# Kernel tuning notes

Hardware: AMD Instinct MI355X
Metric: run time of the kernel (lower is better)

The kernel has to match this reference:

```python
import jax, jax.numpy as jnp
import numpy as np

T, D = 1024, 1024            # tokens, model dim
E, K = 16, 4                 # routed experts, top-k
G, TG = 4, 2                 # expert groups, limited (top) groups
INTER = 512                  # moe_inter_dim
SHARED_INTER = 2 * INTER     # n_shared_experts * moe_inter_dim
ROUTE_SCALE = 2.5
STD = 0.02


def setup_inputs() -> dict:
    key = jax.random.key(0)
    ks = jax.random.split(key, 9)
    return {
        "x": jax.random.normal(ks[0], (T, D), jnp.float32),
        "token_mask": jnp.ones((T,), jnp.bool_),
        "gate_w": jax.random.normal(ks[1], (E, D), jnp.float32) * STD,
        "gate_bias": jnp.zeros((E,), jnp.float32),  # e_score_correction_bias (zero-init)
        "gate_projs": jax.random.normal(ks[2], (E, INTER, D), jnp.float32) * STD,
        "up_projs": jax.random.normal(ks[3], (E, INTER, D), jnp.float32) * STD,
        "down_projs": jax.random.normal(ks[4], (E, D, INTER), jnp.float32) * STD,
        "shared_gate": jax.random.normal(ks[5], (SHARED_INTER, D), jnp.float32) * STD,
        "shared_up": jax.random.normal(ks[6], (SHARED_INTER, D), jnp.float32) * STD,
        "shared_down": jax.random.normal(ks[7], (D, SHARED_INTER), jnp.float32) * STD,
    }


def _route(x, gate_w, gate_bias):
    # sigmoid scoring with e_score_correction_bias + group-limited top-k (DeepSeek-V3 style)
    scores = jax.nn.sigmoid(x @ gate_w.T)                      # [T, E]
    s = (scores + gate_bias).reshape(T, G, E // G)             # bias-corrected, grouped
    group_scores = jax.lax.top_k(s, 2)[0].sum(-1)              # [T, G] sum of top-2 per group
    gidx = jax.lax.top_k(group_scores, TG)[1]                  # [T, TG]
    gmask = jax.nn.one_hot(gidx, G, dtype=s.dtype).sum(1)      # [T, G] selected-group mask
    masked = (s * gmask[:, :, None]).reshape(T, E)
    idx = jax.lax.top_k(masked, K)[1]                          # [T, K] expert indices
    w = jnp.take_along_axis(scores, idx, axis=1)               # gather original (unbiased) scores
    w = w / w.sum(-1, keepdims=True) * ROUTE_SCALE             # sigmoid renorm + route scale
    return w.astype(x.dtype), idx


def reference(x, token_mask, gate_w, gate_bias, gate_projs, up_projs,
              down_projs, shared_gate, shared_up, shared_down):
    w, idx = _route(x, gate_w, gate_bias)
    # dense combine weights [T, E]: combine[t, e] = sum_k w[t, k] * (idx[t, k] == e)
    combine = (jax.nn.one_hot(idx, E, dtype=x.dtype) * w[..., None]).sum(1)

    def body(acc, p):
        gp, up, dp, c = p                                      # per-expert SwiGLU
        inter = jax.nn.silu(x @ gp.T) * (x @ up.T)             # [T, INTER]
        return acc + c[:, None] * (inter @ dp.T), None

    routed, _ = jax.lax.scan(
        body, jnp.zeros_like(x), (gate_projs, up_projs, down_projs, combine.T))
    shared = (jax.nn.silu(x @ shared_gate.T) * (x @ shared_up.T)) @ shared_down.T
    return routed + shared
```

## Files before the change

kernel.cpp:

```cpp
#include <hip/hip_runtime.h>
#include <stdint.h>

#define TTOK 1024
#define DMODEL 1024
#define NEXP 16
#define TOPK 4
#define INTER 512
#define NSHI 1024
#define RSCALE 2.5f

typedef __bf16 bf16;
typedef __bf16 bf16x8 __attribute__((ext_vector_type(8)));
typedef __bf16 bf16x4 __attribute__((ext_vector_type(4)));
typedef float f32x4 __attribute__((ext_vector_type(4)));

#define APLANE 2064
#define BPLANE 1040

__global__ __launch_bounds__(256)
void scores_kernel(const float* __restrict__ x, const float* __restrict__ gw,
                   float* __restrict__ scores, bf16* __restrict__ xbf) {
  __shared__ float gws[16 * 1024];
  const int tid = threadIdx.x;
  const float4* gw4 = (const float4*)gw;
#pragma unroll
  for (int i0 = 0; i0 < 4096; i0 += 256) {
    const int i = i0 + tid;
    const int e = i >> 8;
    const int dq = (i & 255) << 2;
    const int dd = (dq + 4 * e) & 1023;
    ((float4*)gws)[(e << 8) + (dd >> 2)] = gw4[i];
  }
  {
    const long xb = (long)blockIdx.x * 1024;
#pragma unroll
    for (int p = 0; p < 4; ++p) {
      const long j = xb + p * 256 + tid;
      const float4 v = ((const float4*)x)[j];
      bf16x4 o;
      o.x = (bf16)v.x; o.y = (bf16)v.y; o.z = (bf16)v.z; o.w = (bf16)v.w;
      ((bf16x4*)xbf)[j] = o;
    }
  }
  __syncthreads();
  const int kq = tid >> 6;
  const int lane = tid & 63;
  const int tl = lane >> 4;
  const int e = lane & 15;
  const long token = (long)blockIdx.x * 4 + tl;
  float acc = 0.f;
  const int dbase = kq * 256;
#pragma unroll 8
  for (int i = 0; i < 256; i += 4) {
    const int d = dbase + i;
    const float4 xv = *(const float4*)&x[token * DMODEL + d];
    const float4 wv = *(const float4*)&gws[(e << 10) + ((d + 4 * e) & 1023)];
    acc += xv.x * wv.x + xv.y * wv.y + xv.z * wv.z + xv.w * wv.w;
  }
  __syncthreads();
  gws[kq * 64 + lane] = acc;
  __syncthreads();
  if (kq == 0) {
    const float s = gws[lane] + gws[64 + lane] + gws[128 + lane] + gws[192 + lane];
    scores[token * 16 + e] = s;
  }
}

__global__ __launch_bounds__(256)
void topk_kernel(const float* __restrict__ scores, const float* __restrict__ gb,
                 int* __restrict__ tokIdx, float* __restrict__ tokW,
                 int* __restrict__ counts) {
  __shared__ int h[NEXP];
  const int tid = threadIdx.x;
  if (tid < NEXP) h[tid] = 0;
  __syncthreads();
  const int t = blockIdx.x * 256 + tid;
  float sc[NEXP], s[NEXP];
#pragma unroll
  for (int e = 0; e < NEXP; ++e) {
    const float l = scores[t * NEXP + e];
    sc[e] = 1.f / (1.f + expf(-l));
    s[e] = sc[e] + gb[e];
  }
  float gsc[4];
#pragma unroll
  for (int g = 0; g < 4; ++g) {
    const float a = s[4 * g], b = s[4 * g + 1], c = s[4 * g + 2], d = s[4 * g + 3];
    gsc[g] = fmaxf(fmaxf(fmaxf(a + b, a + c), fmaxf(a + d, b + c)),
                   fmaxf(b + d, c + d));
  }
  int g0 = 0;
  for (int g = 1; g < 4; ++g) if (gsc[g] > gsc[g0]) g0 = g;
  int g1 = (g0 == 0) ? 1 : 0;
  for (int g = 0; g < 4; ++g) if (g != g0 && gsc[g] > gsc[g1]) g1 = g;
  float m[NEXP];
#pragma unroll
  for (int e = 0; e < NEXP; ++e) {
    const int g = e >> 2;
    m[e] = (g == g0 || g == g1) ? s[e] : -1.f;
  }
  int idx[TOPK]; float wv[TOPK]; float wsum = 0.f;
  for (int k = 0; k < TOPK; ++k) {
    int am = 0; float best = m[0];
    for (int e2 = 1; e2 < NEXP; ++e2)
      if (m[e2] > best) { best = m[e2]; am = e2; }
    idx[k] = am; wv[k] = sc[am]; wsum += sc[am]; m[am] = -2.f;
  }
  const float scl = RSCALE / wsum;
  for (int k = 0; k < TOPK; ++k) {
    tokIdx[t * TOPK + k] = idx[k];
    tokW[t * TOPK + k] = wv[k] * scl;
    atomicAdd(&h[idx[k]], 1);
  }
  __syncthreads();
  if (tid < NEXP) atomicAdd(&counts[tid], h[tid]);
}

__global__ void plan_kernel(const int* __restrict__ counts, int* __restrict__ offs,
                            int* __restrict__ cursors, int* __restrict__ tileE,
                            int* __restrict__ tileR, int* __restrict__ tileCnt) {
  if (threadIdx.x == 0) {
    int acc = 0;
    for (int e = 0; e < NEXP; ++e) { offs[e] = acc; cursors[e] = acc; acc += counts[e]; }
    offs[NEXP] = acc;
    int tc = 0;
    for (int e = 0; e < NEXP; ++e)
      for (int r = offs[e]; r < offs[e + 1]; r += 128) { tileE[tc] = e; tileR[tc] = r; ++tc; }
    for (int r = 0; r < TTOK; r += 128) { tileE[tc] = NEXP; tileR[tc] = r; ++tc; }
    tileCnt[0] = tc;
  }
}

__global__ __launch_bounds__(256)
void fill_kernel(const int* __restrict__ tokIdx, int* __restrict__ cursors,
                 int* __restrict__ slotTok, int* __restrict__ tokSlot) {
  __shared__ int h[NEXP], base[NEXP];
  const int tid = threadIdx.x;
  if (tid < NEXP) h[tid] = 0;
  __syncthreads();
  const int t = blockIdx.x * 256 + tid;
  int myE[TOPK], myR[TOPK];
#pragma unroll
  for (int k = 0; k < TOPK; ++k) {
    myE[k] = tokIdx[t * TOPK + k];
    myR[k] = atomicAdd(&h[myE[k]], 1);
  }
  __syncthreads();
  if (tid < NEXP) base[tid] = atomicAdd(&cursors[tid], h[tid]);
  __syncthreads();
#pragma unroll
  for (int k = 0; k < TOPK; ++k) {
    const int slot = base[myE[k]] + myR[k];
    slotTok[slot] = t;
    tokSlot[t * TOPK + k] = slot;
  }
}

__global__ __launch_bounds__(256, 2)
void gateup_gemm(const bf16* __restrict__ xbf, const int* __restrict__ slotTok,
                 const int* __restrict__ offs, const int* __restrict__ tileE,
                 const int* __restrict__ tileR, const int* __restrict__ tileCnt,
                 const float* __restrict__ Wg, const float* __restrict__ Wu,
                 const float* __restrict__ Sg, const float* __restrict__ Su,
                 bf16* __restrict__ interR, bf16* __restrict__ interS) {
  const int y = blockIdx.y;
  if (y >= tileCnt[0]) return;
  const int e = tileE[y];
  const bool shd = (e == NEXP);
  const int n0 = blockIdx.x * 64;
  if (!shd && n0 >= INTER) return;
  const int rowStart = tileR[y];
  const int rowEnd = shd ? rowStart + 128 : offs[e + 1];
  const float* wgp = shd ? Sg : Wg + (long)e * INTER * DMODEL;
  const float* wup = shd ? Su : Wu + (long)e * INTER * DMODEL;

  __shared__ __attribute__((aligned(16))) char As[8 * APLANE];
  __shared__ __attribute__((aligned(16))) char Bg[8 * BPLANE];
  __shared__ __attribute__((aligned(16))) char Bu[8 * BPLANE];
  __shared__ int tokS[128];

  const int tid = threadIdx.x;
  if (tid < 128) {
    const int r = rowStart + tid;
    tokS[tid] = shd ? r : slotTok[r < rowEnd ? r : rowStart];
  }
  __syncthreads();

  const int arw = tid >> 3;
  const int aoct = tid & 7;
  const bf16* aSrc[4];
#pragma unroll
  for (int p = 0; p < 4; ++p)
    aSrc[p] = xbf + (long)tokS[p * 32 + arw] * DMODEL + aoct * 8;

  const int bu_ = tid >> 7;
  const int u = tid & 127;
  const int brw = u >> 4;
  const int bf4 = u & 15;
  const int boct = bf4 >> 1;
  const int bhalf = bf4 & 1;
  const float* bSrc = (bu_ ? wup : wgp) + (long)n0 * DMODEL + bf4 * 4;
  char* bDst = bu_ ? Bu : Bg;

  const int lane = tid & 63;
  const int wv = tid >> 6;
  const int q = lane >> 4;
  const int l15 = lane & 15;
  const int wm = (wv >> 1) * 64;
  const int wn = (wv & 1) * 32;

  const f32x4 fz = {0.f, 0.f, 0.f, 0.f};
  f32x4 accG[4][2], accU[4][2];
#pragma unroll
  for (int i = 0; i < 4; ++i)
#pragma unroll
    for (int j = 0; j < 2; ++j) { accG[i][j] = fz; accU[i][j] = fz; }

  bf16x8 av[4];
  float4 bv[8];
#pragma unroll
  for (int p = 0; p < 4; ++p) av[p] = *(const bf16x8*)(aSrc[p]);
#pragma unroll
  for (int p = 0; p < 8; ++p)
    bv[p] = *(const float4*)(bSrc + (long)(p * 8 + brw) * DMODEL);

  for (int k0 = 0; k0 < DMODEL; k0 += 64) {
    __syncthreads();
#pragma unroll
    for (int p = 0; p < 4; ++p)
      *(bf16x8*)(As + aoct * APLANE + (p * 32 + arw) * 16) = av[p];
#pragma unroll
    for (int p = 0; p < 8; ++p) {
      bf16x4 w;
      w.x = (bf16)bv[p].x; w.y = (bf16)bv[p].y; w.z = (bf16)bv[p].z; w.w = (bf16)bv[p].w;
      *(bf16x4*)(bDst + boct * BPLANE + (p * 8 + brw) * 16 + bhalf * 8) = w;
    }
    const int kn = k0 + 64;
    if (kn < DMODEL) {
#pragma unroll
      for (int p = 0; p < 4; ++p) av[p] = *(const bf16x8*)(aSrc[p] + kn);
#pragma unroll
      for (int p = 0; p < 8; ++p)
        bv[p] = *(const float4*)(bSrc + (long)(p * 8 + brw) * DMODEL + kn);
    }
    __syncthreads();
#pragma unroll
    for (int kb = 0; kb < 2; ++kb) {
      bf16x8 aF[4];
#pragma unroll
      for (int mi = 0; mi < 4; ++mi)
        aF[mi] = *(const bf16x8*)(As + (4 * kb + q) * APLANE + (wm + 16 * mi + l15) * 16);
#pragma unroll
      for (int ni = 0; ni < 2; ++ni) {
        const int br = wn + 16 * ni + l15;
        const bf16x8 gF = *(const bf16x8*)(Bg + (4 * kb + q) * BPLANE + br * 16);
        const bf16x8 uF = *(const bf16x8*)(Bu + (4 * kb + q) * BPLANE + br * 16);
#pragma unroll
        for (int mi = 0; mi < 4; ++mi) {
          accG[mi][ni] = __builtin_amdgcn_mfma_f32_16x16x32_bf16(aF[mi], gF, accG[mi][ni], 0, 0, 0);
          accU[mi][ni] = __builtin_amdgcn_mfma_f32_16x16x32_bf16(aF[mi], uF, accU[mi][ni], 0, 0, 0);
        }
      }
    }
  }

  bf16* outI = shd ? interS : interR;
  const int ldI = shd ? NSHI : INTER;
#pragma unroll
  for (int mi = 0; mi < 4; ++mi)
#pragma unroll
    for (int r = 0; r < 4; ++r) {
      const int rowLoc = wm + 16 * mi + q * 4 + r;
      const int row = rowStart + rowLoc;
      if (row < rowEnd) {
#pragma unroll
        for (int ni = 0; ni < 2; ++ni) {
          const float gg = accG[mi][ni][r];
          const float uu = accU[mi][ni][r];
          const float sv = gg / (1.f + __expf(-gg)) * uu;
          outI[(long)row * ldI + (n0 + wn + 16 * ni + l15)] = (bf16)sv;
        }
      }
    }
}

__global__ __launch_bounds__(256, 2)
void down_gemm(const bf16* __restrict__ interR, const bf16* __restrict__ interS,
               const int* __restrict__ offs, const int* __restrict__ tileE,
               const int* __restrict__ tileR, const int* __restrict__ tileCnt,
               const float* __restrict__ Wd, const float* __restrict__ Sd,
               float* __restrict__ dsR, float* __restrict__ dsS) {
  const int y = blockIdx.y;
  if (y >= tileCnt[0]) return;
  const int e = tileE[y];
  const bool shd = (e == NEXP);
  const int n0 = blockIdx.x * 64;
  const int rowStart = tileR[y];
  const int rowEnd = shd ? rowStart + 128 : offs[e + 1];
  const int Kd = shd ? NSHI : INTER;
  const bf16* A = shd ? interS : interR;
  const float* wd = shd ? Sd : Wd + (long)e * DMODEL * INTER;

  __shared__ __attribute__((aligned(16))) char As[8 * APLANE];
  __shared__ __attribute__((aligned(16))) char Bs[8 * BPLANE];

  const int tid = threadIdx.x;
  const int arw = tid >> 3;
  const int aoct = tid & 7;
  const bf16* aSrc[4];
#pragma unroll
  for (int p = 0; p < 4; ++p)
    aSrc[p] = A + (long)(rowStart + p * 32 + arw) * Kd + aoct * 8;

  const int brw = tid >> 4;
  const int bf4 = tid & 15;
  const int boct = bf4 >> 1;
  const int bhalf = bf4 & 1;
  const float* bSrc = wd + (long)n0 * Kd + bf4 * 4;

  const int lane = tid & 63;
  const int wv = tid >> 6;
  const int q = lane >> 4;
  const int l15 = lane & 15;
  const int wm = (wv >> 1) * 64;
  const int wn = (wv & 1) * 32;

  const f32x4 fz = {0.f, 0.f, 0.f, 0.f};
  f32x4 acc[4][2];
#pragma unroll
  for (int i = 0; i < 4; ++i)
#pragma unroll
    for (int j = 0; j < 2; ++j) acc[i][j] = fz;

  bf16x8 av[4];
  float4 bv[4];
#pragma unroll
  for (int p = 0; p < 4; ++p) av[p] = *(const bf16x8*)(aSrc[p]);
#pragma unroll
  for (int p = 0; p < 4; ++p)
    bv[p] = *(const float4*)(bSrc + (long)(p * 16 + brw) * Kd);

  for (int k0 = 0; k0 < Kd; k0 += 64) {
    __syncthreads();
#pragma unroll
    for (int p = 0; p < 4; ++p)
      *(bf16x8*)(As + aoct * APLANE + (p * 32 + arw) * 16) = av[p];
#pragma unroll
    for (int p = 0; p < 4; ++p) {
      bf16x4 w;
      w.x = (bf16)bv[p].x; w.y = (bf16)bv[p].y; w.z = (bf16)bv[p].z; w.w = (bf16)bv[p].w;
      *(bf16x4*)(Bs + boct * BPLANE + (p * 16 + brw) * 16 + bhalf * 8) = w;
    }
    const int kn = k0 + 64;
    if (kn < Kd) {
#pragma unroll
      for (int p = 0; p < 4; ++p) av[p] = *(const bf16x8*)(aSrc[p] + kn);
#pragma unroll
      for (int p = 0; p < 4; ++p)
        bv[p] = *(const float4*)(bSrc + (long)(p * 16 + brw) * Kd + kn);
    }
    __syncthreads();
#pragma unroll
    for (int kb = 0; kb < 2; ++kb) {
      bf16x8 aF[4];
#pragma unroll
      for (int mi = 0; mi < 4; ++mi)
        aF[mi] = *(const bf16x8*)(As + (4 * kb + q) * APLANE + (wm + 16 * mi + l15) * 16);
#pragma unroll
      for (int ni = 0; ni < 2; ++ni) {
        const bf16x8 bF = *(const bf16x8*)(Bs + (4 * kb + q) * BPLANE + (wn + 16 * ni + l15) * 16);
#pragma unroll
        for (int mi = 0; mi < 4; ++mi)
          acc[mi][ni] = __builtin_amdgcn_mfma_f32_16x16x32_bf16(aF[mi], bF, acc[mi][ni], 0, 0, 0);
      }
    }
  }

  float* dst = shd ? dsS : dsR;
#pragma unroll
  for (int mi = 0; mi < 4; ++mi)
#pragma unroll
    for (int r = 0; r < 4; ++r) {
      const int rowLoc = wm + 16 * mi + q * 4 + r;
      const int row = rowStart + rowLoc;
      if (row < rowEnd) {
#pragma unroll
        for (int ni = 0; ni < 2; ++ni)
          dst[(long)row * DMODEL + (n0 + wn + 16 * ni + l15)] = acc[mi][ni][r];
      }
    }
}

__global__ __launch_bounds__(256)
void combine_kernel(const float* __restrict__ dsR, const float* __restrict__ dsS,
                    const int* __restrict__ tokSlot, const float* __restrict__ tokW,
                    float* __restrict__ out) {
  const int t = blockIdx.x;
  const int j = threadIdx.x;
  float4 v = ((const float4*)(dsS + (long)t * DMODEL))[j];
#pragma unroll
  for (int k = 0; k < TOPK; ++k) {
    const int s = tokSlot[t * TOPK + k];
    const float w = tokW[t * TOPK + k];
    const float4 r = ((const float4*)(dsR + (long)s * DMODEL))[j];
    v.x += w * r.x; v.y += w * r.y; v.z += w * r.z; v.w += w * r.w;
  }
  ((float4*)(out + (long)t * DMODEL))[j] = v;
}

extern "C" void kernel_launch(void* const* d_in, const int* in_sizes, int n_in,
                              void* d_out, int out_size, void* d_ws, size_t ws_size,
                              hipStream_t stream) {
  const float* x  = (const float*)d_in[0];
  const float* gw = (const float*)d_in[2];
  const float* gb = (const float*)d_in[3];
  const float* gp = (const float*)d_in[4];
  const float* up = (const float*)d_in[5];
  const float* dp = (const float*)d_in[6];
  const float* sg = (const float*)d_in[7];
  const float* su = (const float*)d_in[8];
  const float* sd = (const float*)d_in[9];
  float* out = (float*)d_out;

  char* base = (char*)d_ws;
  size_t off = 0;
  auto alloc = [&](size_t bytes) -> char* {
    off = (off + 255) & ~(size_t)255;
    char* p = base + off;
    off += bytes;
    return p;
  };
  bf16* xbf = (bf16*)alloc((size_t)TTOK * DMODEL * 2);
  bf16* interR = (bf16*)alloc((size_t)(TTOK * TOPK + 128) * INTER * 2);
  bf16* interS = (bf16*)alloc((size_t)TTOK * NSHI * 2);
  float* dsR = (float*)alloc((size_t)TTOK * TOPK * DMODEL * 4);
  float* dsS = (float*)alloc((size_t)TTOK * DMODEL * 4);
  float* scores = (float*)alloc((size_t)TTOK * NEXP * 4);
  int* tokIdx = (int*)alloc(TTOK * TOPK * 4);
  float* tokW = (float*)alloc(TTOK * TOPK * 4);
  int* slotTok = (int*)alloc(TTOK * TOPK * 4);
  int* tokSlot = (int*)alloc(TTOK * TOPK * 4);
  int* counts = (int*)alloc(NEXP * 4);
  int* offs = (int*)alloc((NEXP + 1) * 4);
  int* cursors = (int*)alloc(NEXP * 4);
  int* tileE = (int*)alloc(72 * 4);
  int* tileR = (int*)alloc(72 * 4);
  int* tileCnt = (int*)alloc(4);

  hipMemsetAsync(counts, 0, NEXP * 4, stream);

  scores_kernel<<<TTOK / 4, 256, 0, stream>>>(x, gw, scores, xbf);
  topk_kernel<<<TTOK / 256, 256, 0, stream>>>(scores, gb, tokIdx, tokW, counts);
  plan_kernel<<<1, 64, 0, stream>>>(counts, offs, cursors, tileE, tileR, tileCnt);
  fill_kernel<<<TTOK / 256, 256, 0, stream>>>(tokIdx, cursors, slotTok, tokSlot);

  gateup_gemm<<<dim3(16, 56, 1), 256, 0, stream>>>(
      xbf, slotTok, offs, tileE, tileR, tileCnt, gp, up, sg, su, interR, interS);
  down_gemm<<<dim3(16, 56, 1), 256, 0, stream>>>(
      interR, interS, offs, tileE, tileR, tileCnt, dp, sd, dsR, dsS);
  combine_kernel<<<TTOK, 256, 0, stream>>>(dsR, dsS, tokSlot, tokW, out);
}
```

Before: 220.9 us.

## Retile MoE GEMMs with double-buffered LDS, direct global-to-LDS loads, and split-K down

The gate/up and down GEMMs move to 256-row tiles with K-step 32 and double-buffered shared memory, so each iteration needs only one barrier. Activation tiles are copied with global_load_lds directly into LDS instead of through registers. The down GEMM now uses 128-wide N tiles and splits K into two halves written to separate buffers, which the combine kernel adds together. This aims to increase reuse and overlap of loads with MFMA work, at the cost of extra workspace, extra combine traffic, and possibly more register pressure under the launch bound of 3.

```diff
diff --git a/kernel.cpp b/kernel.cpp
--- a/kernel.cpp
+++ b/kernel.cpp
@@ -14,8 +14,18 @@
 typedef __bf16 bf16x4 __attribute__((ext_vector_type(4)));
 typedef float f32x4 __attribute__((ext_vector_type(4)));
 
-#define APLANE 2064
-#define BPLANE 1040
+#define APL 4112
+#define BPL32 528
+#define BPL128 2064
+#define ASZ (4 * APL)
+#define BSZ32 (4 * BPL32)
+#define BSZ128 (4 * BPL128)
+
+__device__ __forceinline__ void glds16(void* lds, const void* g) {
+  __builtin_amdgcn_global_load_lds(
+      (const __attribute__((address_space(1))) unsigned int*)g,
+      (__attribute__((address_space(3))) unsigned int*)lds, 16, 0, 0);
+}
 
 __global__ __launch_bounds__(256)
 void scores_kernel(const float* __restrict__ x, const float* __restrict__ gw,
@@ -125,8 +135,8 @@
     offs[NEXP] = acc;
     int tc = 0;
     for (int e = 0; e < NEXP; ++e)
-      for (int r = offs[e]; r < offs[e + 1]; r += 128) { tileE[tc] = e; tileR[tc] = r; ++tc; }
-    for (int r = 0; r < TTOK; r += 128) { tileE[tc] = NEXP; tileR[tc] = r; ++tc; }
+      for (int r = offs[e]; r < offs[e + 1]; r += 256) { tileE[tc] = e; tileR[tc] = r; ++tc; }
+    for (int r = 0; r < TTOK; r += 256) { tileE[tc] = NEXP; tileR[tc] = r; ++tc; }
     tileCnt[0] = tc;
   }
 }
@@ -156,7 +166,7 @@
   }
 }
 
-__global__ __launch_bounds__(256, 2)
+__global__ __launch_bounds__(256, 3)
 void gateup_gemm(const bf16* __restrict__ xbf, const int* __restrict__ slotTok,
                  const int* __restrict__ offs, const int* __restrict__ tileE,
                  const int* __restrict__ tileR, const int* __restrict__ tileCnt,
@@ -167,47 +177,43 @@
   if (y >= tileCnt[0]) return;
   const int e = tileE[y];
   const bool shd = (e == NEXP);
-  const int n0 = blockIdx.x * 64;
+  const int n0 = blockIdx.x * 32;
   if (!shd && n0 >= INTER) return;
   const int rowStart = tileR[y];
-  const int rowEnd = shd ? rowStart + 128 : offs[e + 1];
+  const int rowEnd = shd ? rowStart + 256 : offs[e + 1];
   const float* wgp = shd ? Sg : Wg + (long)e * INTER * DMODEL;
   const float* wup = shd ? Su : Wu + (long)e * INTER * DMODEL;
 
-  __shared__ __attribute__((aligned(16))) char As[8 * APLANE];
-  __shared__ __attribute__((aligned(16))) char Bg[8 * BPLANE];
-  __shared__ __attribute__((aligned(16))) char Bu[8 * BPLANE];
-  __shared__ int tokS[128];
+  __shared__ __attribute__((aligned(16))) char As[2 * ASZ];
+  __shared__ __attribute__((aligned(16))) char Bg[2 * BSZ32];
+  __shared__ __attribute__((aligned(16))) char Bu[2 * BSZ32];
+  __shared__ int tokS[256];
 
   const int tid = threadIdx.x;
-  if (tid < 128) {
+  {
     const int r = rowStart + tid;
-    tokS[tid] = shd ? r : slotTok[r < rowEnd ? r : rowStart];
-  }
-  __syncthreads();
-
-  const int arw = tid >> 3;
-  const int aoct = tid & 7;
-  const bf16* aSrc[4];
-#pragma unroll
-  for (int p = 0; p < 4; ++p)
-    aSrc[p] = xbf + (long)tokS[p * 32 + arw] * DMODEL + aoct * 8;
-
-  const int bu_ = tid >> 7;
-  const int u = tid & 127;
-  const int brw = u >> 4;
-  const int bf4 = u & 15;
-  const int boct = bf4 >> 1;
-  const int bhalf = bf4 & 1;
-  const float* bSrc = (bu_ ? wup : wgp) + (long)n0 * DMODEL + bf4 * 4;
-  char* bDst = bu_ ? Bu : Bg;
+    tokS[tid] = shd ? (r < TTOK ? r : rowStart)
+                    : slotTok[r < rowEnd ? r : rowStart];
+  }
+  __syncthreads();
 
   const int lane = tid & 63;
   const int wv = tid >> 6;
+  const bf16* aG[4];
+#pragma unroll
+  for (int p = 0; p < 4; ++p)
+    aG[p] = xbf + (long)tokS[p * 64 + lane] * DMODEL + wv * 8;
+
+  const int mat = tid >> 7;
+  const int u = tid & 127;
+  const int brow = u >> 2;
+  const int boct = u & 3;
+  const float* bp = (mat ? wup : wgp) + (long)(n0 + brow) * DMODEL + boct * 8;
+  char* bL = (mat ? Bu : Bg);
+
   const int q = lane >> 4;
   const int l15 = lane & 15;
-  const int wm = (wv >> 1) * 64;
-  const int wn = (wv & 1) * 32;
+  const int wm = wv * 64;
 
   const f32x4 fz = {0.f, 0.f, 0.f, 0.f};
   f32x4 accG[4][2], accU[4][2];
@@ -216,50 +222,53 @@
 #pragma unroll
     for (int j = 0; j < 2; ++j) { accG[i][j] = fz; accU[i][j] = fz; }
 
-  bf16x8 av[4];
-  float4 bv[8];
-#pragma unroll
-  for (int p = 0; p < 4; ++p) av[p] = *(const bf16x8*)(aSrc[p]);
-#pragma unroll
-  for (int p = 0; p < 8; ++p)
-    bv[p] = *(const float4*)(bSrc + (long)(p * 8 + brw) * DMODEL);
-
-  for (int k0 = 0; k0 < DMODEL; k0 += 64) {
+  float4 b0 = *(const float4*)(bp);
+  float4 b1 = *(const float4*)(bp + 4);
+  {
+#pragma unroll
+    for (int p = 0; p < 4; ++p)
+      glds16(As + wv * APL + (p * 64) * 16, aG[p]);
+    bf16x8 w;
+    w[0] = (bf16)b0.x; w[1] = (bf16)b0.y; w[2] = (bf16)b0.z; w[3] = (bf16)b0.w;
+    w[4] = (bf16)b1.x; w[5] = (bf16)b1.y; w[6] = (bf16)b1.z; w[7] = (bf16)b1.w;
+    *(bf16x8*)(bL + boct * BPL32 + brow * 16) = w;
+  }
+  b0 = *(const float4*)(bp + 32);
+  b1 = *(const float4*)(bp + 36);
+
+  int buf = 0;
+  for (int k0 = 0; k0 < DMODEL; k0 += 32, buf ^= 1) {
     __syncthreads();
-#pragma unroll
-    for (int p = 0; p < 4; ++p)
-      *(bf16x8*)(As + aoct * APLANE + (p * 32 + arw) * 16) = av[p];
-#pragma unroll
-    for (int p = 0; p < 8; ++p) {
-      bf16x4 w;
-      w.x = (bf16)bv[p].x; w.y = (bf16)bv[p].y; w.z = (bf16)bv[p].z; w.w = (bf16)bv[p].w;
-      *(bf16x4*)(bDst + boct * BPLANE + (p * 8 + brw) * 16 + bhalf * 8) = w;
-    }
-    const int kn = k0 + 64;
+    const int nxt = buf ^ 1;
+    const int kn = k0 + 32;
     if (kn < DMODEL) {
 #pragma unroll
-      for (int p = 0; p < 4; ++p) av[p] = *(const bf16x8*)(aSrc[p] + kn);
-#pragma unroll
-      for (int p = 0; p < 8; ++p)
-        bv[p] = *(const float4*)(bSrc + (long)(p * 8 + brw) * DMODEL + kn);
-    }
-    __syncthreads();
-#pragma unroll
-    for (int kb = 0; kb < 2; ++kb) {
-      bf16x8 aF[4];
-#pragma unroll
-      for (int mi = 0; mi < 4; ++mi)
-        aF[mi] = *(const bf16x8*)(As + (4 * kb + q) * APLANE + (wm + 16 * mi + l15) * 16);
-#pragma unroll
-      for (int ni = 0; ni < 2; ++ni) {
-        const int br = wn + 16 * ni + l15;
-        const bf16x8 gF = *(const bf16x8*)(Bg + (4 * kb + q) * BPLANE + br * 16);
-        const bf16x8 uF = *(const bf16x8*)(Bu + (4 * kb + q) * BPLANE + br * 16);
-#pragma unroll
-        for (int mi = 0; mi < 4; ++mi) {
-          accG[mi][ni] = __builtin_amdgcn_mfma_f32_16x16x32_bf16(aF[mi], gF, accG[mi][ni], 0, 0, 0);
-          accU[mi][ni] = __builtin_amdgcn_mfma_f32_16x16x32_bf16(aF[mi], uF, accU[mi][ni], 0, 0, 0);
-        }
+      for (int p = 0; p < 4; ++p)
+        glds16(As + nxt * ASZ + wv * APL + (p * 64) * 16, aG[p] + kn);
+      bf16x8 w;
+      w[0] = (bf16)b0.x; w[1] = (bf16)b0.y; w[2] = (bf16)b0.z; w[3] = (bf16)b0.w;
+      w[4] = (bf16)b1.x; w[5] = (bf16)b1.y; w[6] = (bf16)b1.z; w[7] = (bf16)b1.w;
+      *(bf16x8*)(bL + nxt * BSZ32 + boct * BPL32 + brow * 16) = w;
+      if (kn + 32 < DMODEL) {
+        b0 = *(const float4*)(bp + kn + 32);
+        b1 = *(const float4*)(bp + kn + 36);
+      }
+    }
+    const char* ab = As + buf * ASZ;
+    const char* gb_ = Bg + buf * BSZ32;
+    const char* ub = Bu + buf * BSZ32;
+    bf16x8 aF[4];
+#pragma unroll
+    for (int mi = 0; mi < 4; ++mi)
+      aF[mi] = *(const bf16x8*)(ab + q * APL + (wm + 16 * mi + l15) * 16);
+#pragma unroll
+    for (int ni = 0; ni < 2; ++ni) {
+      const bf16x8 gF = *(const bf16x8*)(gb_ + q * BPL32 + (16 * ni + l15) * 16);
+      const bf16x8 uF = *(const bf16x8*)(ub + q * BPL32 + (16 * ni + l15) * 16);
+#pragma unroll
+      for (int mi = 0; mi < 4; ++mi) {
+        accG[mi][ni] = __builtin_amdgcn_mfma_f32_16x16x32_bf16(aF[mi], gF, accG[mi][ni], 0, 0, 0);
+        accU[mi][ni] = __builtin_amdgcn_mfma_f32_16x16x32_bf16(aF[mi], uF, accU[mi][ni], 0, 0, 0);
       }
     }
   }
@@ -278,7 +287,7 @@
           const float gg = accG[mi][ni][r];
           const float uu = accU[mi][ni][r];
           const float sv = gg / (1.f + __expf(-gg)) * uu;
-          outI[(long)row * ldI + (n0 + wn + 16 * ni + l15)] = (bf16)sv;
+          outI[(long)row * ldI + (n0 + 16 * ni + l15)] = (bf16)sv;
         }
       }
     }
@@ -289,94 +298,108 @@
                const int* __restrict__ offs, const int* __restrict__ tileE,
                const int* __restrict__ tileR, const int* __restrict__ tileCnt,
                const float* __restrict__ Wd, const float* __restrict__ Sd,
-               float* __restrict__ dsR, float* __restrict__ dsS) {
+               float* __restrict__ dsR0, float* __restrict__ dsR1,
+               float* __restrict__ dsS0, float* __restrict__ dsS1) {
   const int y = blockIdx.y;
   if (y >= tileCnt[0]) return;
+  const int ks = blockIdx.z;
   const int e = tileE[y];
   const bool shd = (e == NEXP);
-  const int n0 = blockIdx.x * 64;
+  const int n0 = blockIdx.x * 128;
   const int rowStart = tileR[y];
-  const int rowEnd = shd ? rowStart + 128 : offs[e + 1];
-  const int Kd = shd ? NSHI : INTER;
+  const int rowEnd = shd ? rowStart + 256 : offs[e + 1];
+  const int KdF = shd ? NSHI : INTER;
+  const int Kh = KdF >> 1;
+  const int kb = ks * Kh;
   const bf16* A = shd ? interS : interR;
   const float* wd = shd ? Sd : Wd + (long)e * DMODEL * INTER;
 
-  __shared__ __attribute__((aligned(16))) char As[8 * APLANE];
-  __shared__ __attribute__((aligned(16))) char Bs[8 * BPLANE];
+  __shared__ __attribute__((aligned(16))) char As[2 * ASZ];
+  __shared__ __attribute__((aligned(16))) char Bs[2 * BSZ128];
 
   const int tid = threadIdx.x;
-  const int arw = tid >> 3;
-  const int aoct = tid & 7;
-  const bf16* aSrc[4];
-#pragma unroll
-  for (int p = 0; p < 4; ++p)
-    aSrc[p] = A + (long)(rowStart + p * 32 + arw) * Kd + aoct * 8;
-
-  const int brw = tid >> 4;
-  const int bf4 = tid & 15;
-  const int boct = bf4 >> 1;
-  const int bhalf = bf4 & 1;
-  const float* bSrc = wd + (long)n0 * Kd + bf4 * 4;
-
   const int lane = tid & 63;
   const int wv = tid >> 6;
+  const bf16* aG[4];
+#pragma unroll
+  for (int p = 0; p < 4; ++p)
+    aG[p] = A + (long)(rowStart + p * 64 + lane) * KdF + kb + wv * 8;
+
+  const int brow = tid >> 1;
+  const int h2 = tid & 1;
+  const float* bp = wd + (long)(n0 + brow) * KdF + kb + h2 * 16;
+
   const int q = lane >> 4;
   const int l15 = lane & 15;
-  const int wm = (wv >> 1) * 64;
-  const int wn = (wv & 1) * 32;
+  const int wm = wv * 64;
 
   const f32x4 fz = {0.f, 0.f, 0.f, 0.f};
-  f32x4 acc[4][2];
+  f32x4 acc[4][8];
 #pragma unroll
   for (int i = 0; i < 4; ++i)
 #pragma unroll
-    for (int j = 0; j < 2; ++j) acc[i][j] = fz;
-
-  bf16x8 av[4];
-  float4 bv[4];
-#pragma unroll
-  for (int p = 0; p < 4; ++p) av[p] = *(const bf16x8*)(aSrc[p]);
-#pragma unroll
-  for (int p = 0; p < 4; ++p)
-    bv[p] = *(const float4*)(bSrc + (long)(p * 16 + brw) * Kd);
-
-  for (int k0 = 0; k0 < Kd; k0 += 64) {
+    for (int j = 0; j < 8; ++j) acc[i][j] = fz;
+
+  float4 bv0, bv1, bv2, bv3;
+#define DN_LOADB(K0)                      \
+  {                                       \
+    bv0 = *(const float4*)(bp + (K0));    \
+    bv1 = *(const float4*)(bp + (K0) + 4);  \
+    bv2 = *(const float4*)(bp + (K0) + 8);  \
+    bv3 = *(const float4*)(bp + (K0) + 12); \
+  }
+#define DN_WRITEB(BASE)                                                    \
+  {                                                                        \
+    bf16x4 w0, w1, w2, w3;                                                 \
+    w0[0] = (bf16)bv0.x; w0[1] = (bf16)bv0.y; w0[2] = (bf16)bv0.z; w0[3] = (bf16)bv0.w; \
+    w1[0] = (bf16)bv1.x; w1[1] = (bf16)bv1.y; w1[2] = (bf16)bv1.z; w1[3] = (bf16)bv1.w; \
+    w2[0] = (bf16)bv2.x; w2[1] = (bf16)bv2.y; w2[2] = (bf16)bv2.z; w2[3] = (bf16)bv2.w; \
+    w3[0] = (bf16)bv3.x; w3[1] = (bf16)bv3.y; w3[2] = (bf16)bv3.z; w3[3] = (bf16)bv3.w; \
+    *(bf16x4*)((BASE) + (h2 * 2 + 0) * BPL128 + brow * 16 + 0) = w0;       \
+    *(bf16x4*)((BASE) + (h2 * 2 + 0) * BPL128 + brow * 16 + 8) = w1;       \
+    *(bf16x4*)((BASE) + (h2 * 2 + 1) * BPL128 + brow * 16 + 0) = w2;       \
+    *(bf16x4*)((BASE) + (h2 * 2 + 1) * BPL128 + brow * 16 + 8) = w3;       \
+  }
+
+  DN_LOADB(0);
+  {
+#pragma unroll
+    for (int p = 0; p < 4; ++p)
+      glds16(As + wv * APL + (p * 64) * 16, aG[p]);
+    DN_WRITEB(Bs);
+  }
+  DN_LOADB(32);
+
+  int buf = 0;
+  for (int k0 = 0; k0 < Kh; k0 += 32, buf ^= 1) {
     __syncthreads();
-#pragma unroll
-    for (int p = 0; p < 4; ++p)
-      *(bf16x8*)(As + aoct * APLANE + (p * 32 + arw) * 16) = av[p];
-#pragma unroll
-    for (int p = 0; p < 4; ++p) {
-      bf16x4 w;
-      w.x = (bf16)bv[p].x; w.y = (bf16)bv[p].y; w.z = (bf16)bv[p].z; w.w = (bf16)bv[p].w;
-      *(bf16x4*)(Bs + boct * BPLANE + (p * 16 + brw) * 16 + bhalf * 8) = w;
-    }
-    const int kn = k0 + 64;
-    if (kn < Kd) {
-#pragma unroll
-      for (int p = 0; p < 4; ++p) av[p] = *(const bf16x8*)(aSrc[p] + kn);
+    const int nxt = buf ^ 1;
+    const int kn = k0 + 32;
+    if (kn < Kh) {
 #pragma unroll
       for (int p = 0; p < 4; ++p)
-        bv[p] = *(const float4*)(bSrc + (long)(p * 16 + brw) * Kd + kn);
-    }
-    __syncthreads();
-#pragma unroll
-    for (int kb = 0; kb < 2; ++kb) {
-      bf16x8 aF[4];
+        glds16(As + nxt * ASZ + wv * APL + (p * 64) * 16, aG[p] + kn);
+      DN_WRITEB(Bs + nxt * BSZ128);
+      if (kn + 32 < Kh) DN_LOADB(kn + 32);
+    }
+    const char* ab = As + buf * ASZ;
+    const char* bb = Bs + buf * BSZ128;
+    bf16x8 aF[4];
+#pragma unroll
+    for (int mi = 0; mi < 4; ++mi)
+      aF[mi] = *(const bf16x8*)(ab + q * APL + (wm + 16 * mi + l15) * 16);
+#pragma unroll
+    for (int ni = 0; ni < 8; ++ni) {
+      const bf16x8 bF = *(const bf16x8*)(bb + q * BPL128 + (16 * ni + l15) * 16);
 #pragma unroll
       for (int mi = 0; mi < 4; ++mi)
-        aF[mi] = *(const bf16x8*)(As + (4 * kb + q) * APLANE + (wm + 16 * mi + l15) * 16);
-#pragma unroll
-      for (int ni = 0; ni < 2; ++ni) {
-        const bf16x8 bF = *(const bf16x8*)(Bs + (4 * kb + q) * BPLANE + (wn + 16 * ni + l15) * 16);
-#pragma unroll
-        for (int mi = 0; mi < 4; ++mi)
-          acc[mi][ni] = __builtin_amdgcn_mfma_f32_16x16x32_bf16(aF[mi], bF, acc[mi][ni], 0, 0, 0);
-      }
-    }
-  }
-
-  float* dst = shd ? dsS : dsR;
+        acc[mi][ni] = __builtin_amdgcn_mfma_f32_16x16x32_bf16(aF[mi], bF, acc[mi][ni], 0, 0, 0);
+    }
+  }
+#undef DN_LOADB
+#undef DN_WRITEB
+
+  float* dst = shd ? (ks ? dsS1 : dsS0) : (ks ? dsR1 : dsR0);
 #pragma unroll
   for (int mi = 0; mi < 4; ++mi)
 #pragma unroll
@@ -385,27 +408,35 @@
       const int row = rowStart + rowLoc;
       if (row < rowEnd) {
 #pragma unroll
-        for (int ni = 0; ni < 2; ++ni)
-          dst[(long)row * DMODEL + (n0 + wn + 16 * ni + l15)] = acc[mi][ni][r];
+        for (int ni = 0; ni < 8; ++ni)
+          dst[(long)row * DMODEL + (n0 + 16 * ni + l15)] = acc[mi][ni][r];
       }
     }
 }
 
 __global__ __launch_bounds__(256)
-void combine_kernel(const float* __restrict__ dsR, const float* __restrict__ dsS,
+void combine_kernel(const float* __restrict__ dsR0, const float* __restrict__ dsR1,
+                    const float* __restrict__ dsS0, const float* __restrict__ dsS1,
                     const int* __restrict__ tokSlot, const float* __restrict__ tokW,
                     float* __restrict__ out) {
   const int t = blockIdx.x;
   const int j = threadIdx.x;
-  float4 v = ((const float4*)(dsS + (long)t * DMODEL))[j];
+  const long o = (long)t * 256 + j;
+  const float4 s0 = ((const float4*)dsS0)[o];
+  const float4 s1 = ((const float4*)dsS1)[o];
+  float4 v;
+  v.x = s0.x + s1.x; v.y = s0.y + s1.y; v.z = s0.z + s1.z; v.w = s0.w + s1.w;
 #pragma unroll
   for (int k = 0; k < TOPK; ++k) {
     const int s = tokSlot[t * TOPK + k];
     const float w = tokW[t * TOPK + k];
-    const float4 r = ((const float4*)(dsR + (long)s * DMODEL))[j];
-    v.x += w * r.x; v.y += w * r.y; v.z += w * r.z; v.w += w * r.w;
-  }
-  ((float4*)(out + (long)t * DMODEL))[j] = v;
+    const long so = (long)s * 256 + j;
+    const float4 r0 = ((const float4*)dsR0)[so];
+    const float4 r1 = ((const float4*)dsR1)[so];
+    v.x += w * (r0.x + r1.x); v.y += w * (r0.y + r1.y);
+    v.z += w * (r0.z + r1.z); v.w += w * (r0.w + r1.w);
+  }
+  ((float4*)out)[o] = v;
 }
 
 extern "C" void kernel_launch(void* const* d_in, const int* in_sizes, int n_in,
@@ -430,11 +461,14 @@
     off += bytes;
     return p;
   };
+  const int PADSLOTS = TTOK * TOPK + 256;
   bf16* xbf = (bf16*)alloc((size_t)TTOK * DMODEL * 2);
-  bf16* interR = (bf16*)alloc((size_t)(TTOK * TOPK + 128) * INTER * 2);
+  bf16* interR = (bf16*)alloc((size_t)PADSLOTS * INTER * 2);
   bf16* interS = (bf16*)alloc((size_t)TTOK * NSHI * 2);
-  float* dsR = (float*)alloc((size_t)TTOK * TOPK * DMODEL * 4);
-  float* dsS = (float*)alloc((size_t)TTOK * DMODEL * 4);
+  float* dsR0 = (float*)alloc((size_t)PADSLOTS * DMODEL * 4);
+  float* dsR1 = (float*)alloc((size_t)PADSLOTS * DMODEL * 4);
+  float* dsS0 = (float*)alloc((size_t)TTOK * DMODEL * 4);
+  float* dsS1 = (float*)alloc((size_t)TTOK * DMODEL * 4);
   float* scores = (float*)alloc((size_t)TTOK * NEXP * 4);
   int* tokIdx = (int*)alloc(TTOK * TOPK * 4);
   float* tokW = (float*)alloc(TTOK * TOPK * 4);
@@ -454,9 +488,9 @@
   plan_kernel<<<1, 64, 0, stream>>>(counts, offs, cursors, tileE, tileR, tileCnt);
   fill_kernel<<<TTOK / 256, 256, 0, stream>>>(tokIdx, cursors, slotTok, tokSlot);
 
-  gateup_gemm<<<dim3(16, 56, 1), 256, 0, stream>>>(
+  gateup_gemm<<<dim3(32, 36, 1), 256, 0, stream>>>(
       xbf, slotTok, offs, tileE, tileR, tileCnt, gp, up, sg, su, interR, interS);
-  down_gemm<<<dim3(16, 56, 1), 256, 0, stream>>>(
-      interR, interS, offs, tileE, tileR, tileCnt, dp, sd, dsR, dsS);
-  combine_kernel<<<TTOK, 256, 0, stream>>>(dsR, dsS, tokSlot, tokW, out);
-}
+  down_gemm<<<dim3(8, 36, 2), 256, 0, stream>>>(
+      interR, interS, offs, tileE, tileR, tileCnt, dp, sd, dsR0, dsR1, dsS0, dsS1);
+  combine_kernel<<<TTOK, 256, 0, stream>>>(dsR0, dsR1, dsS0, dsS1, tokSlot, tokW, out);
+}
```

After: 293.0 us. 32.7% more time.
